# Kernel tuning notes

Hardware: AMD Instinct MI355X
Metric: run time of the kernel (lower is better)

Reference implementation:

```python
import jax, jax.numpy as jnp
import numpy as np

N_USERS = 100000
N_ITEMS = 50000
N_NODES = N_USERS + N_ITEMS
NNZ = 4800000
EMB = 64
N_LAYERS = 3
BATCH = 4096
REG = 1e-5


def setup_inputs() -> dict:
    key = jax.random.key(0)
    ks = jax.random.split(key, 12)
    rows = jax.random.randint(ks[0], (NNZ,), 0, N_NODES, dtype=jnp.int32)
    cols = jax.random.randint(ks[1], (NNZ,), 0, N_NODES, dtype=jnp.int32)
    # normalized-Laplacian-like positive edge weights
    vals = jax.random.uniform(ks[2], (NNZ,), dtype=jnp.float32) * 0.05
    user_emb = jax.random.normal(ks[3], (N_USERS, EMB), dtype=jnp.float32) * 0.1
    item_emb = jax.random.normal(ks[4], (N_ITEMS, EMB), dtype=jnp.float32) * 0.1
    # xavier-ish scale for 64x64: std ~= 0.125
    W_one = jax.random.normal(ks[5], (N_LAYERS, EMB, EMB), dtype=jnp.float32) * 0.125
    b_one = jax.random.normal(ks[6], (N_LAYERS, EMB), dtype=jnp.float32) * 0.125
    W_two = jax.random.normal(ks[7], (N_LAYERS, EMB, EMB), dtype=jnp.float32) * 0.125
    b_two = jax.random.normal(ks[8], (N_LAYERS, EMB), dtype=jnp.float32) * 0.125
    u = jax.random.randint(ks[9], (BATCH,), 0, N_USERS, dtype=jnp.int32)
    i = jax.random.randint(ks[10], (BATCH,), 0, N_ITEMS, dtype=jnp.int32)
    j = jax.random.randint(ks[11], (BATCH,), 0, N_ITEMS, dtype=jnp.int32)
    return {"rows": rows, "cols": cols, "vals": vals, "user_emb": user_emb,
            "item_emb": item_emb, "W_one": W_one, "b_one": b_one,
            "W_two": W_two, "b_two": b_two, "u": u, "i": i, "j": j}


def _spmm(rows, cols, vals, x):
    # sparse.mm(L, x): gather rows of x at cols, scale by edge vals, scatter-add into rows
    return jax.ops.segment_sum(vals[:, None] * x[cols], rows, num_segments=N_NODES)


def reference(rows, cols, vals, user_emb, item_emb, W_one, b_one, W_two, b_two, u, i, j):
    ego = jnp.concatenate([user_emb, item_emb], axis=0)  # [N_NODES, EMB]
    finals = [ego]
    for k in range(N_LAYERS):
        xk = finals[k]
        side_L = _spmm(rows, cols, vals, xk)          # L @ x
        side_LI = side_L + xk                          # (L + I) @ x
        simple = side_LI @ W_one[k] + b_one[k]
        interaction = (side_L * xk) @ W_two[k] + b_two[k]
        ego_k = jax.nn.leaky_relu(simple + interaction)  # mess_dropout=0 -> identity
        norm = ego_k / jnp.maximum(jnp.linalg.norm(ego_k, axis=1, keepdims=True), 1e-12)
        finals.append(norm)
    final = jnp.concatenate(finals, axis=1)            # [N_NODES, EMB*(1+N_LAYERS)]
    u_emb = final[u]
    p_emb = final[N_USERS + i]
    n_emb = final[N_USERS + j]
    y_ui = jnp.sum(u_emb * p_emb, axis=1)
    y_uj = jnp.sum(u_emb * n_emb, axis=1)
    bpr_loss = -jnp.mean(jax.nn.log_sigmoid(y_ui - y_uj))
    l2norm = (jnp.sum(u_emb ** 2) / 2.0 + jnp.sum(p_emb ** 2) / 2.0 + jnp.sum(n_emb ** 2) / 2.0) / BATCH
    return bpr_loss + REG * l2norm
```

## Files before the change

kernel.cpp:

```cpp
#include <hip/hip_runtime.h>
#include <hip/hip_bf16.h>
#include <math.h>

#define N_USERS 100000
#define N_ITEMS 50000
#define N_NODES 150000
#define NNZ     4800000
#define EMB     64
#define BATCH   4096
#define REG_C   1e-5f

#define ROWB    512
#define NBK     293
#define PADC    17408
#define CSTRIDE 16
#define P1_EPB  2048
#define NB_P1   ((NNZ + P1_EPB - 1) / P1_EPB)
#define NB_PACK 2344
#define NB_ACC0 1024

#define LROW    36

typedef short short8 __attribute__((ext_vector_type(8)));
typedef float f32x4  __attribute__((ext_vector_type(4)));
typedef float f32x2  __attribute__((ext_vector_type(2)));
typedef unsigned uint32x4 __attribute__((ext_vector_type(4)));

static __device__ __forceinline__ unsigned short f2bf(float f) {
    unsigned u = __float_as_uint(f);
    u = u + 0x7FFFu + ((u >> 16) & 1u);
    return (unsigned short)(u >> 16);
}
static __device__ __forceinline__ unsigned pk2(float lo, float hi) {
    return (unsigned)f2bf(lo) | ((unsigned)f2bf(hi) << 16);
}
static __device__ __forceinline__ float blo(unsigned a) { return __uint_as_float(a << 16); }
static __device__ __forceinline__ float bhi(unsigned a) { return __uint_as_float(a & 0xFFFF0000u); }

static __device__ __forceinline__ unsigned pkq4(float f0, float f1, float f2, float f3) {
    int v = __builtin_amdgcn_cvt_pk_fp8_f32(f0, f1, 0, false);
    v = __builtin_amdgcn_cvt_pk_fp8_f32(f2, f3, v, true);
    return (unsigned)v;
}

static __device__ __forceinline__ void eload(const int2* p_, int& c, float& v) {
    unsigned long long w = __builtin_nontemporal_load((const unsigned long long*)p_);
    c = (int)(unsigned)(w & 0xFFFFFFFFu);
    v = __int_as_float((int)(unsigned)(w >> 32));
}
static __device__ __forceinline__ int ntl(const int* p_) {
    return __builtin_nontemporal_load(p_);
}
static __device__ __forceinline__ float ntlf(const float* p_) {
    return __builtin_nontemporal_load(p_);
}
static __device__ __forceinline__ uint32x4 ntl4(const unsigned* p_) {
    return __builtin_nontemporal_load((const uint32x4*)p_);
}

static __device__ __forceinline__ void ldsbar() {
    __builtin_amdgcn_sched_barrier(0);
    asm volatile("s_waitcnt lgkmcnt(0)" ::: "memory");
    __builtin_amdgcn_s_barrier();
    __builtin_amdgcn_sched_barrier(0);
}

__global__ __launch_bounds__(256) void p1_bin_kernel(
    const int* __restrict__ rows, const int* __restrict__ cols,
    const float* __restrict__ vals, int* __restrict__ gcursor,
    int2* __restrict__ binned,
    const float* __restrict__ ue, const float* __restrict__ ie,
    unsigned int* __restrict__ xh, unsigned int* __restrict__ xq,
    const int* __restrict__ u, const int* __restrict__ ii,
    const int* __restrict__ jj,
    float* __restrict__ dui, float* __restrict__ duj, float* __restrict__ l2a) {
    __shared__ int2 staged[P1_EPB];
    __shared__ unsigned char bkt[P1_EPB];
    __shared__ int hist[NBK];
    __shared__ int lofs[NBK];
    __shared__ int baseg[NBK];
    int t = threadIdx.x;
    int bid = blockIdx.x;

    if (bid >= NB_P1 + NB_PACK) {
        int b = (bid - NB_P1 - NB_PACK) * 4 + (t >> 6);
        int lane = t & 63;
        float uv = ue[(size_t)u[b] * 64 + lane];
        float pv = ie[(size_t)ii[b] * 64 + lane];
        float nv = ie[(size_t)jj[b] * 64 + lane];
        float a = uv * pv, c = uv * nv, l = uv * uv + pv * pv + nv * nv;
        #pragma unroll
        for (int o = 32; o > 0; o >>= 1) {
            a += __shfl_xor(a, o, 64);
            c += __shfl_xor(c, o, 64);
            l += __shfl_xor(l, o, 64);
        }
        if (lane == 0) { dui[b] = a; duj[b] = c; l2a[b] = l; }
        return;
    }
    if (bid >= NB_P1) {
        int g0 = ((bid - NB_P1) * 256 + t) * 2;
        #pragma unroll
        for (int g = g0; g < g0 + 2; ++g) {
            if (g >= N_NODES * 8) break;
            const float4* src;
            if (g < N_USERS * 8) src = (const float4*)ue + (size_t)g * 2;
            else src = (const float4*)ie + (size_t)(g - N_USERS * 8) * 2;
            float4 a = src[0], b = src[1];
            uint4 h;
            h.x = pk2(a.x, a.y); h.y = pk2(a.z, a.w);
            h.z = pk2(b.x, b.y); h.w = pk2(b.z, b.w);
            ((uint4*)xh)[g] = h;
            uint2 q;
            q.x = pkq4(a.x, a.y, a.z, a.w);
            q.y = pkq4(b.x, b.y, b.z, b.w);
            ((uint2*)xq)[g] = q;
        }
        return;
    }

    int e0 = bid * P1_EPB;
    int nE = NNZ - e0; if (nE > P1_EPB) nE = P1_EPB;
    int wv = t >> 6, l = t & 63;

    for (int b = t; b < NBK; b += 256) hist[b] = 0;
    ldsbar();
    for (int i = t; i < nE; i += 256) atomicAdd(&hist[rows[e0 + i] >> 9], 1);
    ldsbar();

    int bA = t, bB = t + 256;
    int hA = (bA < NBK) ? hist[bA] : 0;
    int hB = (bB < NBK) ? hist[bB] : 0;
    int resA = 0, resB = 0;
    if (hA > 0) resA = atomicAdd(&gcursor[bA * CSTRIDE], hA);
    if (hB > 0) resB = atomicAdd(&gcursor[bB * CSTRIDE], hB);
    if (wv == 0) {
        int carry = 0;
        #pragma unroll
        for (int c = 0; c < 5; ++c) {
            int idx = c * 64 + l;
            int v = (idx < NBK) ? hist[idx] : 0;
            int x = v;
            #pragma unroll
            for (int o = 1; o < 64; o <<= 1) {
                int y = __shfl_up(x, o, 64);
                if (l >= o) x += y;
            }
            if (idx < NBK) lofs[idx] = carry + x - v;
            carry += __shfl(x, 63, 64);
        }
    }
    ldsbar();

    for (int i = t; i < nE; i += 256) {
        int r = rows[e0 + i];
        int bb = r >> 9;
        int rk = atomicAdd(&hist[bb], -1);
        int slot = lofs[bb] + rk - 1;
        staged[slot] = make_int2(ntl(&cols[e0 + i]) | ((r & 511) << 18),
                                 __float_as_int(ntlf(&vals[e0 + i])));
        bkt[slot] = (unsigned char)bb;
    }
    if (bA < NBK) baseg[bA] = resA;
    if (bB < NBK) baseg[bB] = resB;
    ldsbar();

    int L256 = lofs[256];
    for (int s = t; s < nE; s += 256) {
        int2 rec = staged[s];
        int bb = (int)bkt[s] + ((s >= L256) ? 256 : 0);
        int rel = baseg[bb] + (s - lofs[bb]);
        if (rel < PADC)
            binned[(size_t)bb * PADC + rel] = rec;
    }
}

__global__ __launch_bounds__(1024) void p2_sort_kernel(
    const int* __restrict__ gcursor, const int2* __restrict__ binned,
    int2* __restrict__ csr, int* __restrict__ start, int* __restrict__ cnt) {
    __shared__ int hist[ROWB];
    __shared__ int excl[ROWB];
    __shared__ int chunk[16];
    int b = blockIdx.x;
    int t = threadIdx.x;
    int wv = t >> 6, l = t & 63;
    size_t bbase = (size_t)b * PADC;
    int n = gcursor[b * CSTRIDE];
    if (n > PADC) n = PADC;
    if (t < ROWB) hist[t] = 0;
    ldsbar();
    for (int i = t; i < n; i += 1024)
        atomicAdd(&hist[(binned[bbase + i].x >> 18) & 511], 1);
    ldsbar();
    int incl = 0;
    if (t < ROWB) {
        incl = hist[t];
        #pragma unroll
        for (int o = 1; o < 64; o <<= 1) {
            int y = __shfl_up(incl, o, 64);
            if (l >= o) incl += y;
        }
        if (l == 63) chunk[wv] = incl;
    }
    ldsbar();
    if (t < ROWB) {
        int add = 0;
        #pragma unroll
        for (int c = 0; c < 8; ++c) add += (c < wv) ? chunk[c] : 0;
        int s = incl + add - hist[t];
        int rowsInB = N_NODES - b * ROWB;
        if (rowsInB > ROWB) rowsInB = ROWB;
        if (t < rowsInB) {
            start[b * ROWB + t] = (int)bbase + s;
            cnt[b * ROWB + t]   = hist[t];
        }
        excl[t] = s;
    }
    ldsbar();
    for (int i = t; i < n; i += 1024) {
        int2 rec = binned[bbase + i];
        int rl = (rec.x >> 18) & 511;
        int p = atomicAdd(&excl[rl], 1);
        csr[bbase + p] = make_int2(rec.x & 0x3FFFF, rec.y);
    }
}

__global__ __launch_bounds__(256) void spmm_csr_kernel(
    const int* __restrict__ start, const int* __restrict__ cnt,
    const int2* __restrict__ edges, const unsigned int* __restrict__ xq,
    unsigned int* __restrict__ out) {
    int row = blockIdx.x * 4 + (threadIdx.x >> 6);
    if (row >= N_NODES) return;
    int lane = threadIdx.x & 63;
    int eg = lane >> 4;
    int p  = lane & 15;
    int s = start[row];
    int n = cnt[row];
    float a0 = 0.f, a1 = 0.f, a2 = 0.f, a3 = 0.f;
    int k = 0;
    for (; k + 32 <= n; k += 32) {
        int c[8]; float v[8];
        #pragma unroll
        for (int j = 0; j < 8; ++j) eload(&edges[s + k + 4 * j + eg], c[j], v[j]);
        #pragma unroll
        for (int j = 0; j < 8; ++j) {
            unsigned q = xq[(size_t)c[j] * 16 + p];
            f32x2 lo = __builtin_amdgcn_cvt_pk_f32_fp8(q, false);
            f32x2 hi = __builtin_amdgcn_cvt_pk_f32_fp8(q, true);
            a0 = fmaf(v[j], lo[0], a0);
            a1 = fmaf(v[j], lo[1], a1);
            a2 = fmaf(v[j], hi[0], a2);
            a3 = fmaf(v[j], hi[1], a3);
        }
    }
    while (k < n) {
        #pragma unroll
        for (int j = 0; j < 4; ++j) {
            int off = k + 4 * j + eg;
            bool valid = off < n;
            int c; float v;
            eload(&edges[s + (valid ? off : 0)], c, v);
            if (!valid) v = 0.f;
            unsigned q = xq[(size_t)c * 16 + p];
            f32x2 lo = __builtin_amdgcn_cvt_pk_f32_fp8(q, false);
            f32x2 hi = __builtin_amdgcn_cvt_pk_f32_fp8(q, true);
            a0 = fmaf(v, lo[0], a0);
            a1 = fmaf(v, lo[1], a1);
            a2 = fmaf(v, hi[0], a2);
            a3 = fmaf(v, hi[1], a3);
        }
        k += 16;
    }
    a0 += __shfl_xor(a0, 16, 64); a0 += __shfl_xor(a0, 32, 64);
    a1 += __shfl_xor(a1, 16, 64); a1 += __shfl_xor(a1, 32, 64);
    a2 += __shfl_xor(a2, 16, 64); a2 += __shfl_xor(a2, 32, 64);
    a3 += __shfl_xor(a3, 16, 64); a3 += __shfl_xor(a3, 32, 64);
    if (eg == 0) {
        uint2 o2;
        o2.x = pk2(a0, a1);
        o2.y = pk2(a2, a3);
        ((uint2*)out)[(size_t)row * 16 + p] = o2;
    }
}

__global__ __launch_bounds__(256) void dense_kernel(
    unsigned int* xh, unsigned int* xq, const unsigned int* __restrict__ sideL,
    const float* __restrict__ W1, const float* __restrict__ b1,
    const float* __restrict__ W2, const float* __restrict__ b2)
{
    __shared__ unsigned asl[64 * LROW];
    __shared__ unsigned apr[64 * LROW];
    __shared__ unsigned wt1[64 * LROW];
    __shared__ unsigned wt2[64 * LROW];

    int t = threadIdx.x;
    int r0 = blockIdx.x * 64;

    #pragma unroll
    for (int i = 0; i < 4; ++i) {
        int idx = i * 256 + t;
        int kk = idx >> 4;
        int ng = idx & 15;
        float4 w1v = ((const float4*)W1)[idx];
        float4 w2v = ((const float4*)W2)[idx];
        unsigned short* s1 = (unsigned short*)wt1;
        unsigned short* s2 = (unsigned short*)wt2;
        int c0 = 4 * ng;
        s1[(c0 + 0) * (2 * LROW) + kk] = f2bf(w1v.x);
        s1[(c0 + 1) * (2 * LROW) + kk] = f2bf(w1v.y);
        s1[(c0 + 2) * (2 * LROW) + kk] = f2bf(w1v.z);
        s1[(c0 + 3) * (2 * LROW) + kk] = f2bf(w1v.w);
        s2[(c0 + 0) * (2 * LROW) + kk] = f2bf(w2v.x);
        s2[(c0 + 1) * (2 * LROW) + kk] = f2bf(w2v.y);
        s2[(c0 + 2) * (2 * LROW) + kk] = f2bf(w2v.z);
        s2[(c0 + 3) * (2 * LROW) + kk] = f2bf(w2v.w);
    }

    #pragma unroll
    for (int i = 0; i < 2; ++i) {
        int q = i * 256 + t;
        int row = q >> 3;
        int u4 = q & 7;
        uint4 h  = make_uint4(0, 0, 0, 0);
        uint32x4 sb = {0u, 0u, 0u, 0u};
        if (r0 + row < N_NODES) {
            h  = ((const uint4*)xh)[(size_t)(r0 + row) * 8 + u4];
            sb = ntl4(sideL + ((size_t)(r0 + row) * 8 + u4) * 4);
        }
        float x0 = blo(h.x), x1 = bhi(h.x), x2 = blo(h.y), x3 = bhi(h.y);
        float x4 = blo(h.z), x5 = bhi(h.z), x6 = blo(h.w), x7 = bhi(h.w);
        float d0 = blo(sb.x), d1 = bhi(sb.x), d2 = blo(sb.y), d3 = bhi(sb.y);
        float d4 = blo(sb.z), d5 = bhi(sb.z), d6 = blo(sb.w), d7 = bhi(sb.w);
        uint4 sa, pa;
        sa.x = pk2(x0 + d0, x1 + d1); sa.y = pk2(x2 + d2, x3 + d3);
        sa.z = pk2(x4 + d4, x5 + d5); sa.w = pk2(x6 + d6, x7 + d7);
        pa.x = pk2(x0 * d0, x1 * d1); pa.y = pk2(x2 * d2, x3 * d3);
        pa.z = pk2(x4 * d4, x5 * d5); pa.w = pk2(x6 * d6, x7 * d7);
        *(uint4*)&asl[row * LROW + 4 * u4] = sa;
        *(uint4*)&apr[row * LROW + 4 * u4] = pa;
    }
    __syncthreads();

    int l = t & 63, wv = t >> 6;
    int q4 = l >> 4, mr = l & 15;
    int abase = (wv * 16 + mr) * LROW + 4 * q4;
    short8 aS0 = *(const short8*)&asl[abase];
    short8 aS1 = *(const short8*)&asl[abase + 16];
    short8 aP0 = *(const short8*)&apr[abase];
    short8 aP1 = *(const short8*)&apr[abase + 16];

    float lr[4][4];
    float rowss[4] = {0.f, 0.f, 0.f, 0.f};
    #pragma unroll
    for (int nb = 0; nb < 4; ++nb) {
        int wbase = (nb * 16 + mr) * LROW + 4 * q4;
        short8 b10 = *(const short8*)&wt1[wbase];
        short8 b11 = *(const short8*)&wt1[wbase + 16];
        short8 b20 = *(const short8*)&wt2[wbase];
        short8 b21 = *(const short8*)&wt2[wbase + 16];
        f32x4 acc = {0.f, 0.f, 0.f, 0.f};
        acc = __builtin_amdgcn_mfma_f32_16x16x32_bf16(aS0, b10, acc, 0, 0, 0);
        acc = __builtin_amdgcn_mfma_f32_16x16x32_bf16(aS1, b11, acc, 0, 0, 0);
        acc = __builtin_amdgcn_mfma_f32_16x16x32_bf16(aP0, b20, acc, 0, 0, 0);
        acc = __builtin_amdgcn_mfma_f32_16x16x32_bf16(aP1, b21, acc, 0, 0, 0);
        float bias = b1[nb * 16 + mr] + b2[nb * 16 + mr];
        #pragma unroll
        for (int r = 0; r < 4; ++r) {
            float v = acc[r] + bias;
            float lrv = v > 0.f ? v : 0.01f * v;
            lr[nb][r] = lrv;
            rowss[r] += lrv * lrv;
        }
    }
    #pragma unroll
    for (int o = 1; o < 16; o <<= 1) {
        #pragma unroll
        for (int r = 0; r < 4; ++r) rowss[r] += __shfl_xor(rowss[r], o, 64);
    }
    float inv[4];
    #pragma unroll
    for (int r = 0; r < 4; ++r) inv[r] = 1.f / fmaxf(sqrtf(rowss[r]), 1e-12f);

    __syncthreads();
    unsigned short* os = (unsigned short*)wt1;
    #pragma unroll
    for (int nb = 0; nb < 4; ++nb) {
        #pragma unroll
        for (int r = 0; r < 4; ++r) {
            int rloc = wv * 16 + q4 * 4 + r;
            os[rloc * (2 * LROW) + nb * 16 + mr] = f2bf(lr[nb][r] * inv[r]);
        }
    }
    __syncthreads();

    #pragma unroll
    for (int i = 0; i < 2; ++i) {
        int q = i * 256 + t;
        int row = q >> 3, u4 = q & 7;
        if (r0 + row < N_NODES) {
            uint4 h = *(const uint4*)&wt1[row * LROW + 4 * u4];
            ((uint4*)xh)[(size_t)(r0 + row) * 8 + u4] = h;
            uint2 qq;
            qq.x = pkq4(blo(h.x), bhi(h.x), blo(h.y), bhi(h.y));
            qq.y = pkq4(blo(h.z), bhi(h.z), blo(h.w), bhi(h.w));
            ((uint2*)xq)[(size_t)(r0 + row) * 8 + u4] = qq;
        }
    }
}

__global__ void accB_kernel(const unsigned int* __restrict__ xh,
                            const int* __restrict__ u, const int* __restrict__ ii,
                            const int* __restrict__ jj,
                            float* __restrict__ dui, float* __restrict__ duj,
                            float* __restrict__ l2a) {
    int t = threadIdx.x;
    int lane = t & 63;
    int half = lane >> 5, p = lane & 31;
    int b = blockIdx.x * 8 + (t >> 6) * 2 + half;
    unsigned ua = xh[(size_t)u[b] * 32 + p];
    unsigned pa = xh[(size_t)(N_USERS + ii[b]) * 32 + p];
    unsigned na = xh[(size_t)(N_USERS + jj[b]) * 32 + p];
    float u0 = blo(ua), u1 = bhi(ua);
    float p0 = blo(pa), p1 = bhi(pa);
    float n0 = blo(na), n1 = bhi(na);
    float a = u0 * p0 + u1 * p1;
    float c = u0 * n0 + u1 * n1;
    float l = u0 * u0 + u1 * u1 + p0 * p0 + p1 * p1 + n0 * n0 + n1 * n1;
    #pragma unroll
    for (int o = 16; o > 0; o >>= 1) {
        a += __shfl_xor(a, o, 64);
        c += __shfl_xor(c, o, 64);
        l += __shfl_xor(l, o, 64);
    }
    if (p == 0) { dui[b] += a; duj[b] += c; l2a[b] += l; }
}

__global__ void final_kernel(const float* __restrict__ dui, const float* __restrict__ duj,
                             const float* __restrict__ l2a, float* __restrict__ out) {
    __shared__ float sh[4];
    int t = threadIdx.x;
    float s = 0.f;
    for (int b = t; b < BATCH; b += 256) {
        float diff = dui[b] - duj[b];
        float ls = (diff >= 0.f) ? -log1pf(expf(-diff)) : (diff - log1pf(expf(diff)));
        s += -ls + REG_C * 0.5f * l2a[b];
    }
    #pragma unroll
    for (int o = 32; o > 0; o >>= 1) s += __shfl_xor(s, o, 64);
    int wave = t >> 6, lane = t & 63;
    if (lane == 0) sh[wave] = s;
    __syncthreads();
    if (t == 0) out[0] = (sh[0] + sh[1] + sh[2] + sh[3]) / (float)BATCH;
}

extern "C" void kernel_launch(void* const* d_in, const int* in_sizes, int n_in,
                              void* d_out, int out_size, void* d_ws, size_t ws_size,
                              hipStream_t stream) {
    const int*   rows     = (const int*)d_in[0];
    const int*   cols     = (const int*)d_in[1];
    const float* vals     = (const float*)d_in[2];
    const float* user_emb = (const float*)d_in[3];
    const float* item_emb = (const float*)d_in[4];
    const float* W_one    = (const float*)d_in[5];
    const float* b_one    = (const float*)d_in[6];
    const float* W_two    = (const float*)d_in[7];
    const float* b_two    = (const float*)d_in[8];
    const int*   u        = (const int*)d_in[9];
    const int*   ii       = (const int*)d_in[10];
    const int*   jj       = (const int*)d_in[11];

    unsigned int* Xh  = (unsigned int*)d_ws;
    unsigned int* Xq  = Xh + (size_t)N_NODES * 32;
    int2* binned      = (int2*)(Xq + (size_t)N_NODES * 16);
    unsigned int* B   = (unsigned int*)binned;
    int2* csr         = binned + (size_t)NBK * PADC;
    int*  gcursor     = (int*)(csr + (size_t)NBK * PADC);
    int*  startA      = gcursor + NBK * CSTRIDE;
    int*  cntA        = startA + 150016;
    float* dui        = (float*)(cntA + 150016);
    float* duj        = dui + BATCH;
    float* l2a        = duj + BATCH;

    (void)hipMemsetAsync(gcursor, 0, NBK * CSTRIDE * sizeof(int), stream);

    p1_bin_kernel<<<NB_P1 + NB_PACK + NB_ACC0, 256, 0, stream>>>(
        rows, cols, vals, gcursor, binned,
        user_emb, item_emb, Xh, Xq, u, ii, jj, dui, duj, l2a);
    p2_sort_kernel<<<NBK, 1024, 0, stream>>>(gcursor, binned, csr, startA, cntA);

    for (int k = 0; k < 3; ++k) {
        spmm_csr_kernel<<<(N_NODES + 3) / 4, 256, 0, stream>>>(startA, cntA, csr, Xq, B);
        dense_kernel<<<(N_NODES + 63) / 64, 256, 0, stream>>>(
            Xh, Xq, B, W_one + k * 4096, b_one + k * 64,
            W_two + k * 4096, b_two + k * 64);
        accB_kernel<<<BATCH / 8, 256, 0, stream>>>(Xh, u, ii, jj, dui, duj, l2a);
    }

    final_kernel<<<1, 256, 0, stream>>>(dui, duj, l2a, (float*)d_out);
}
```

Measured before the change: 601.8 us.

## Fuse batch accumulation into SpMM, pre-pack weights once, use persistent SpMM grid

```diff
diff --git a/kernel.cpp b/kernel.cpp
--- a/kernel.cpp
+++ b/kernel.cpp
@@ -19,6 +19,9 @@
 #define NB_PACK 2344
 #define NB_ACC0 1024
 
+#define SPMM_NB    2048
+#define SPMM_WAVES (SPMM_NB * 4)
+
 #define LROW    36
 
 typedef short short8 __attribute__((ext_vector_type(8)));
@@ -73,7 +76,9 @@
     unsigned int* __restrict__ xh, unsigned int* __restrict__ xq,
     const int* __restrict__ u, const int* __restrict__ ii,
     const int* __restrict__ jj,
-    float* __restrict__ dui, float* __restrict__ duj, float* __restrict__ l2a) {
+    float* __restrict__ dui, float* __restrict__ duj, float* __restrict__ l2a,
+    const float* __restrict__ W1g, const float* __restrict__ W2g,
+    unsigned int* __restrict__ gwt) {
     __shared__ int2 staged[P1_EPB];
     __shared__ unsigned char bkt[P1_EPB];
     __shared__ int hist[NBK];
@@ -82,6 +87,20 @@
     int t = threadIdx.x;
     int bid = blockIdx.x;
 
+    if (bid == NB_P1 + NB_PACK + NB_ACC0) {
+        for (int i = 0; i < 6 * 64 * 32; i += 256) {
+            int e = i + t;
+            int m = e >> 11;
+            int r = e & 2047;
+            int n = r >> 5;
+            int kp = r & 31;
+            const float* Wm = (m < 3) ? (W1g + m * 4096) : (W2g + (m - 3) * 4096);
+            float lo = Wm[(2 * kp) * 64 + n];
+            float hi = Wm[(2 * kp + 1) * 64 + n];
+            gwt[(size_t)m * (64 * LROW) + n * LROW + kp] = pk2(lo, hi);
+        }
+        return;
+    }
     if (bid >= NB_P1 + NB_PACK) {
         int b = (bid - NB_P1 - NB_PACK) * 4 + (t >> 6);
         int lane = t & 63;
@@ -225,68 +244,98 @@
     }
 }
 
-__global__ __launch_bounds__(256) void spmm_csr_kernel(
+__global__ __launch_bounds__(256, 8) void spmm_csr_kernel(
     const int* __restrict__ start, const int* __restrict__ cnt,
     const int2* __restrict__ edges, const unsigned int* __restrict__ xq,
-    unsigned int* __restrict__ out) {
-    int row = blockIdx.x * 4 + (threadIdx.x >> 6);
-    if (row >= N_NODES) return;
-    int lane = threadIdx.x & 63;
+    unsigned int* __restrict__ out,
+    const unsigned int* __restrict__ xh,
+    const int* __restrict__ u, const int* __restrict__ ii,
+    const int* __restrict__ jj,
+    float* __restrict__ dui, float* __restrict__ duj,
+    float* __restrict__ l2a) {
+    int bid = blockIdx.x;
+    int t = threadIdx.x;
+    if (bid >= SPMM_NB) {
+        int lane = t & 63;
+        int half = lane >> 5, pp = lane & 31;
+        int b = (bid - SPMM_NB) * 8 + (t >> 6) * 2 + half;
+        unsigned ua = xh[(size_t)u[b] * 32 + pp];
+        unsigned pa = xh[(size_t)(N_USERS + ii[b]) * 32 + pp];
+        unsigned na = xh[(size_t)(N_USERS + jj[b]) * 32 + pp];
+        float u0 = blo(ua), u1 = bhi(ua);
+        float p0 = blo(pa), p1 = bhi(pa);
+        float n0 = blo(na), n1 = bhi(na);
+        float a = u0 * p0 + u1 * p1;
+        float c = u0 * n0 + u1 * n1;
+        float l = u0 * u0 + u1 * u1 + p0 * p0 + p1 * p1 + n0 * n0 + n1 * n1;
+        #pragma unroll
+        for (int o = 16; o > 0; o >>= 1) {
+            a += __shfl_xor(a, o, 64);
+            c += __shfl_xor(c, o, 64);
+            l += __shfl_xor(l, o, 64);
+        }
+        if (pp == 0) { dui[b] += a; duj[b] += c; l2a[b] += l; }
+        return;
+    }
+    int lane = t & 63;
     int eg = lane >> 4;
     int p  = lane & 15;
-    int s = start[row];
-    int n = cnt[row];
-    float a0 = 0.f, a1 = 0.f, a2 = 0.f, a3 = 0.f;
-    int k = 0;
-    for (; k + 32 <= n; k += 32) {
-        int c[8]; float v[8];
-        #pragma unroll
-        for (int j = 0; j < 8; ++j) eload(&edges[s + k + 4 * j + eg], c[j], v[j]);
-        #pragma unroll
-        for (int j = 0; j < 8; ++j) {
-            unsigned q = xq[(size_t)c[j] * 16 + p];
-            f32x2 lo = __builtin_amdgcn_cvt_pk_f32_fp8(q, false);
-            f32x2 hi = __builtin_amdgcn_cvt_pk_f32_fp8(q, true);
-            a0 = fmaf(v[j], lo[0], a0);
-            a1 = fmaf(v[j], lo[1], a1);
-            a2 = fmaf(v[j], hi[0], a2);
-            a3 = fmaf(v[j], hi[1], a3);
-        }
-    }
-    while (k < n) {
-        #pragma unroll
-        for (int j = 0; j < 4; ++j) {
-            int off = k + 4 * j + eg;
-            bool valid = off < n;
-            int c; float v;
-            eload(&edges[s + (valid ? off : 0)], c, v);
-            if (!valid) v = 0.f;
-            unsigned q = xq[(size_t)c * 16 + p];
-            f32x2 lo = __builtin_amdgcn_cvt_pk_f32_fp8(q, false);
-            f32x2 hi = __builtin_amdgcn_cvt_pk_f32_fp8(q, true);
-            a0 = fmaf(v, lo[0], a0);
-            a1 = fmaf(v, lo[1], a1);
-            a2 = fmaf(v, hi[0], a2);
-            a3 = fmaf(v, hi[1], a3);
-        }
-        k += 16;
-    }
-    a0 += __shfl_xor(a0, 16, 64); a0 += __shfl_xor(a0, 32, 64);
-    a1 += __shfl_xor(a1, 16, 64); a1 += __shfl_xor(a1, 32, 64);
-    a2 += __shfl_xor(a2, 16, 64); a2 += __shfl_xor(a2, 32, 64);
-    a3 += __shfl_xor(a3, 16, 64); a3 += __shfl_xor(a3, 32, 64);
-    if (eg == 0) {
-        uint2 o2;
-        o2.x = pk2(a0, a1);
-        o2.y = pk2(a2, a3);
-        ((uint2*)out)[(size_t)row * 16 + p] = o2;
+    int wave = bid * 4 + (t >> 6);
+    for (int row = wave; row < N_NODES; row += SPMM_WAVES) {
+        int s = start[row];
+        int n = cnt[row];
+        float a0 = 0.f, a1 = 0.f, a2 = 0.f, a3 = 0.f;
+        int k = 0;
+        for (; k + 32 <= n; k += 32) {
+            int c[8]; float v[8];
+            #pragma unroll
+            for (int j = 0; j < 8; ++j) eload(&edges[s + k + 4 * j + eg], c[j], v[j]);
+            #pragma unroll
+            for (int j = 0; j < 8; ++j) {
+                unsigned q = xq[(size_t)c[j] * 16 + p];
+                f32x2 lo = __builtin_amdgcn_cvt_pk_f32_fp8(q, false);
+                f32x2 hi = __builtin_amdgcn_cvt_pk_f32_fp8(q, true);
+                a0 = fmaf(v[j], lo[0], a0);
+                a1 = fmaf(v[j], lo[1], a1);
+                a2 = fmaf(v[j], hi[0], a2);
+                a3 = fmaf(v[j], hi[1], a3);
+            }
+        }
+        while (k < n) {
+            #pragma unroll
+            for (int j = 0; j < 4; ++j) {
+                int off = k + 4 * j + eg;
+                bool valid = off < n;
+                int c; float v;
+                eload(&edges[s + (valid ? off : 0)], c, v);
+                if (!valid) v = 0.f;
+                unsigned q = xq[(size_t)c * 16 + p];
+                f32x2 lo = __builtin_amdgcn_cvt_pk_f32_fp8(q, false);
+                f32x2 hi = __builtin_amdgcn_cvt_pk_f32_fp8(q, true);
+                a0 = fmaf(v, lo[0], a0);
+                a1 = fmaf(v, lo[1], a1);
+                a2 = fmaf(v, hi[0], a2);
+                a3 = fmaf(v, hi[1], a3);
+            }
+            k += 16;
+        }
+        a0 += __shfl_xor(a0, 16, 64); a0 += __shfl_xor(a0, 32, 64);
+        a1 += __shfl_xor(a1, 16, 64); a1 += __shfl_xor(a1, 32, 64);
+        a2 += __shfl_xor(a2, 16, 64); a2 += __shfl_xor(a2, 32, 64);
+        a3 += __shfl_xor(a3, 16, 64); a3 += __shfl_xor(a3, 32, 64);
+        if (eg == 0) {
+            uint2 o2;
+            o2.x = pk2(a0, a1);
+            o2.y = pk2(a2, a3);
+            ((uint2*)out)[(size_t)row * 16 + p] = o2;
+        }
     }
 }
 
 __global__ __launch_bounds__(256) void dense_kernel(
     unsigned int* xh, unsigned int* xq, const unsigned int* __restrict__ sideL,
-    const float* __restrict__ W1, const float* __restrict__ b1,
-    const float* __restrict__ W2, const float* __restrict__ b2)
+    const unsigned int* __restrict__ gw1, const unsigned int* __restrict__ gw2,
+    const float* __restrict__ b1, const float* __restrict__ b2)
 {
     __shared__ unsigned asl[64 * LROW];
     __shared__ unsigned apr[64 * LROW];
@@ -297,23 +346,10 @@
     int r0 = blockIdx.x * 64;
 
     #pragma unroll
-    for (int i = 0; i < 4; ++i) {
+    for (int i = 0; i < 9; ++i) {
         int idx = i * 256 + t;
-        int kk = idx >> 4;
-        int ng = idx & 15;
-        float4 w1v = ((const float4*)W1)[idx];
-        float4 w2v = ((const float4*)W2)[idx];
-        unsigned short* s1 = (unsigned short*)wt1;
-        unsigned short* s2 = (unsigned short*)wt2;
-        int c0 = 4 * ng;
-        s1[(c0 + 0) * (2 * LROW) + kk] = f2bf(w1v.x);
-        s1[(c0 + 1) * (2 * LROW) + kk] = f2bf(w1v.y);
-        s1[(c0 + 2) * (2 * LROW) + kk] = f2bf(w1v.z);
-        s1[(c0 + 3) * (2 * LROW) + kk] = f2bf(w1v.w);
-        s2[(c0 + 0) * (2 * LROW) + kk] = f2bf(w2v.x);
-        s2[(c0 + 1) * (2 * LROW) + kk] = f2bf(w2v.y);
-        s2[(c0 + 2) * (2 * LROW) + kk] = f2bf(w2v.z);
-        s2[(c0 + 3) * (2 * LROW) + kk] = f2bf(w2v.w);
+        wt1[idx] = gw1[idx];
+        wt2[idx] = gw2[idx];
     }
 
     #pragma unroll
@@ -480,21 +516,25 @@
     float* dui        = (float*)(cntA + 150016);
     float* duj        = dui + BATCH;
     float* l2a        = duj + BATCH;
+    unsigned int* gwt = (unsigned int*)(l2a + BATCH);
 
     (void)hipMemsetAsync(gcursor, 0, NBK * CSTRIDE * sizeof(int), stream);
 
-    p1_bin_kernel<<<NB_P1 + NB_PACK + NB_ACC0, 256, 0, stream>>>(
+    p1_bin_kernel<<<NB_P1 + NB_PACK + NB_ACC0 + 1, 256, 0, stream>>>(
         rows, cols, vals, gcursor, binned,
-        user_emb, item_emb, Xh, Xq, u, ii, jj, dui, duj, l2a);
+        user_emb, item_emb, Xh, Xq, u, ii, jj, dui, duj, l2a,
+        W_one, W_two, gwt);
     p2_sort_kernel<<<NBK, 1024, 0, stream>>>(gcursor, binned, csr, startA, cntA);
 
     for (int k = 0; k < 3; ++k) {
-        spmm_csr_kernel<<<(N_NODES + 3) / 4, 256, 0, stream>>>(startA, cntA, csr, Xq, B);
+        int grid = SPMM_NB + ((k > 0) ? (BATCH / 8) : 0);
+        spmm_csr_kernel<<<grid, 256, 0, stream>>>(
+            startA, cntA, csr, Xq, B, Xh, u, ii, jj, dui, duj, l2a);
         dense_kernel<<<(N_NODES + 63) / 64, 256, 0, stream>>>(
-            Xh, Xq, B, W_one + k * 4096, b_one + k * 64,
-            W_two + k * 4096, b_two + k * 64);
-        accB_kernel<<<BATCH / 8, 256, 0, stream>>>(Xh, u, ii, jj, dui, duj, l2a);
-    }
+            Xh, Xq, B, gwt + (size_t)k * 64 * LROW, gwt + (size_t)(3 + k) * 64 * LROW,
+            b_one + k * 64, b_two + k * 64);
+    }
+    accB_kernel<<<BATCH / 8, 256, 0, stream>>>(Xh, u, ii, jj, dui, duj, l2a);
 
     final_kernel<<<1, 256, 0, stream>>>(dui, duj, l2a, (float*)d_out);
 }
```

Measured after the change: 654.9 us. +8.8%, slower.
